# Optimization experiments

Measured on AMD Instinct MI355X. Metric: run time of the kernel, lower is better.

The kernel has to match this reference:

```python
import jax, jax.numpy as jnp
import numpy as np

B, N, C = 16, 2048, 256
C4 = C // 4
BN_EPS = 1e-5


def setup_inputs() -> dict:
    key = jax.random.key(0)
    ks = jax.random.split(key, 9)
    return {
        "x": jax.random.normal(ks[0], (B, N, C), jnp.float32),
        "Wq": jax.random.normal(ks[1], (C4, C), jnp.float32) * (1.0 / np.sqrt(C)),
        "Wk": jax.random.normal(ks[2], (C4, C), jnp.float32) * (1.0 / np.sqrt(C)),
        "Wv": jax.random.normal(ks[3], (C, C), jnp.float32) * (1.0 / np.sqrt(C)),
        "bv": jax.random.normal(ks[4], (C,), jnp.float32) * 0.01,
        "Wt": jax.random.normal(ks[5], (C, C), jnp.float32) * (1.0 / np.sqrt(C)),
        "bt": jax.random.normal(ks[6], (C,), jnp.float32) * 0.01,
        "gamma": jnp.ones((C,), jnp.float32),
        "beta": jnp.zeros((C,), jnp.float32),
        "bn_mean": jax.random.normal(ks[7], (C,), jnp.float32) * 0.1,
        "bn_var": jax.random.uniform(ks[8], (C,), jnp.float32, 0.5, 1.5),
    }


def reference(x, Wq, Wk, Wv, bv, Wt, bt, gamma, beta, bn_mean, bn_var):
    # x: (B, N, C) -> channel-first (B, C, N) as in the torch module
    xc = jnp.transpose(x, (0, 2, 1))                       # (B, C, N)
    q = jnp.einsum('oc,bcn->bno', Wq, xc)                  # (B, N, C4)
    k = jnp.einsum('oc,bcn->bon', Wk, xc)                  # (B, C4, N)
    # v_conv is computed in the original module but its output is never used;
    # it does not affect the forward output.
    energy = jnp.einsum('bno,bom->bnm', q, k)              # (B, N, N)
    attn = jax.nn.softmax(energy, axis=-1)
    # offset-attention double normalization: divide by column sums
    attn = attn / (1e-6 + jnp.sum(attn, axis=1, keepdims=True))
    x_r = jnp.einsum('bcn,bnm->bcm', xc, attn)             # (B, C, N)
    d = xc - x_r
    t = jnp.einsum('oc,bcn->bon', Wt, d) + bt[None, :, None]
    bn = gamma[None, :, None] * (t - bn_mean[None, :, None]) \
         * jax.lax.rsqrt(bn_var[None, :, None] + BN_EPS) + beta[None, :, None]
    out = xc + jnp.maximum(bn, 0.0)                        # residual + ReLU
    return jnp.transpose(out, (0, 2, 1))                   # (B, N, C)
```

## Files before the change

kernel.cpp:

```cpp
#include <hip/hip_runtime.h>
#include <math.h>
#include <stdint.h>

constexpr int B_ = 16, N_ = 2048, C_ = 256, K_ = 64;
constexpr float EPS_BN = 1e-5f;

typedef __attribute__((ext_vector_type(8))) short short8;
typedef __attribute__((ext_vector_type(16))) float f32x16;

#define MFMA32(A, Bf, Cc) __builtin_amdgcn_mfma_f32_32x32x16_bf16(A, Bf, Cc, 0, 0, 0)

constexpr size_t SZ_QK  = (size_t)B_*N_*K_*2;
constexpr size_t WSB_QH = 0;
constexpr size_t WSB_QL = WSB_QH + SZ_QK;
constexpr size_t WSB_KH = WSB_QL + SZ_QK;
constexpr size_t WSB_KL = WSB_KH + SZ_QK;
constexpr size_t WSB_Z  = WSB_KL + SZ_QK;
constexpr size_t WSB_WQT= WSB_Z  + (size_t)B_*N_*4;
constexpr size_t WSB_WKT= WSB_WQT+ (size_t)C_*K_*4;
constexpr size_t WSB_S  = WSB_WKT+ (size_t)C_*K_*4;
constexpr size_t WSB_CB = WSB_S  + (size_t)C_*4;
constexpr size_t WSB_WBH= WSB_CB + (size_t)C_*4;
constexpr size_t WSB_WBL= WSB_WBH+ (size_t)C_*C_*2;
constexpr size_t WSB_XT = (WSB_WBL + (size_t)C_*C_*2 + 255) & ~(size_t)255;
constexpr size_t XT_HALF= (size_t)B_*N_*C_*2;

__device__ inline unsigned short bf16_rne(float f) {
  uint32_t u = __float_as_uint(f);
  uint32_t r = u + 0x7FFFu + ((u >> 16) & 1u);
  return (unsigned short)(r >> 16);
}

#define GLOAD_LDS16(g, l) __builtin_amdgcn_global_load_lds( \
    (const __attribute__((address_space(1))) unsigned int*)(g), \
    (__attribute__((address_space(3))) unsigned int*)(l), 16, 0, 0)

__global__ void k0_prep(const float* __restrict__ Wq, const float* __restrict__ Wk,
                        const float* __restrict__ Wt, const float* __restrict__ bt,
                        const float* __restrict__ gamma, const float* __restrict__ beta,
                        const float* __restrict__ mean, const float* __restrict__ var,
                        char* __restrict__ ws) {
  int o = blockIdx.x, c = threadIdx.x;
  {
    float w = Wt[(size_t)o*C_ + c];
    uint32_t wb = __float_as_uint(w) & 0xFFFF0000u;
    ((unsigned short*)(ws + WSB_WBH))[(size_t)o*C_ + c] = (unsigned short)(wb >> 16);
    ((unsigned short*)(ws + WSB_WBL))[(size_t)o*C_ + c] = bf16_rne(w - __uint_as_float(wb));
  }
  if (o < K_) {
    ((float*)(ws + WSB_WQT))[(size_t)c*K_ + o] = Wq[(size_t)o*C_ + c];
    ((float*)(ws + WSB_WKT))[(size_t)c*K_ + o] = Wk[(size_t)o*C_ + c];
  }
  if (o == 0) {
    float s = gamma[c] * rsqrtf(var[c] + EPS_BN);
    ((float*)(ws + WSB_S))[c]  = s;
    ((float*)(ws + WSB_CB))[c] = s * (bt[c] - mean[c]) + beta[c];
  }
}

__global__ __launch_bounds__(256) void k1_qk(const float* __restrict__ x,
                                             char* __restrict__ ws,
                                             char* __restrict__ xtbuf) {
  __shared__ float xs[32][260];
  const float* WqT = (const float*)(ws + WSB_WQT);
  const float* WkT = (const float*)(ws + WSB_WKT);
  unsigned short* qh = (unsigned short*)(ws + WSB_QH);
  unsigned short* ql = (unsigned short*)(ws + WSB_QL);
  unsigned short* kh = (unsigned short*)(ws + WSB_KH);
  unsigned short* kl = (unsigned short*)(ws + WSB_KL);
  int b = blockIdx.x >> 6, nt = blockIdx.x & 63;
  int n0 = nt * 32, tid = threadIdx.x;

  const float4* xg = (const float4*)(x + ((size_t)b*N_ + n0)*C_);
#pragma unroll
  for (int i = 0; i < 8; i++) {
    int f = tid + i*256;
    int r = f >> 6, c4 = f & 63;
    *(float4*)&xs[r][c4*4] = xg[f];
  }
  __syncthreads();

  int o = tid & 63, rg = tid >> 6;
  float aq[8], ak[8];
#pragma unroll
  for (int j = 0; j < 8; j++) { aq[j] = 0.f; ak[j] = 0.f; }
  for (int c = 0; c < C_; c++) {
    float wq = WqT[c*K_ + o];
    float wk = WkT[c*K_ + o];
#pragma unroll
    for (int j = 0; j < 8; j++) {
      float xv = xs[rg*8 + j][c];
      aq[j] = fmaf(xv, wq, aq[j]);
      ak[j] = fmaf(xv, wk, ak[j]);
    }
  }
#pragma unroll
  for (int j = 0; j < 8; j++) {
    int n = n0 + rg*8 + j;
    size_t base = ((size_t)b*N_ + n)*K_ + o;
    float q = aq[j];
    uint32_t qb = __float_as_uint(q) & 0xFFFF0000u;
    qh[base] = (unsigned short)(qb >> 16);
    ql[base] = bf16_rne(q - __uint_as_float(qb));
    float k = ak[j];
    uint32_t kb = __float_as_uint(k) & 0xFFFF0000u;
    kh[base] = (unsigned short)(kb >> 16);
    kl[base] = bf16_rne(k - __uint_as_float(kb));
  }
#pragma unroll
  for (int nc = 0; nc < 4; nc++) {
    uint32_t hw[4], lw[4];
#pragma unroll
    for (int jj = 0; jj < 4; jj++) {
      float a  = xs[nc*8 + jj*2    ][tid];
      float bv = xs[nc*8 + jj*2 + 1][tid];
      uint32_t ab = __float_as_uint(a)  & 0xFFFF0000u;
      uint32_t bb = __float_as_uint(bv) & 0xFFFF0000u;
      hw[jj] = (ab >> 16) | bb;
      float alo = a  - __uint_as_float(ab);
      float blo = bv - __uint_as_float(bb);
      lw[jj] = (uint32_t)bf16_rne(alo) | ((uint32_t)bf16_rne(blo) << 16);
    }
    size_t toff = ((size_t)(b*64 + nt))*16384 + ((size_t)nc*256 + tid)*16;
    *(uint4*)(xtbuf + toff)           = make_uint4(hw[0], hw[1], hw[2], hw[3]);
    *(uint4*)(xtbuf + XT_HALF + toff) = make_uint4(lw[0], lw[1], lw[2], lw[3]);
  }
}

__global__ __launch_bounds__(256) void k3_stats(char* __restrict__ ws) {
  int b = blockIdx.x >> 4, nb = blockIdx.x & 15;
  int tid = threadIdx.x, wave = tid >> 6, l = tid & 63;
  int lo5 = l & 31, hi5 = l >> 5;
  int n = nb*128 + wave*32 + lo5;

  short8 qhf[4], qlf[4];
  size_t qoff = ((size_t)b*N_ + n)*K_;
#pragma unroll
  for (int cs = 0; cs < 4; cs++) {
    qhf[cs] = *(const short8*)(ws + WSB_QH + (qoff + cs*16 + hi5*8)*2);
    qlf[cs] = *(const short8*)(ws + WSB_QL + (qoff + cs*16 + hi5*8)*2);
  }
  float M = -3.0e38f, S = 0.f;
  for (int mt = 0; mt < 64; mt++) {
    size_t koff = ((size_t)b*N_ + mt*32 + lo5)*K_;
    short8 khf[4], klf[4];
#pragma unroll
    for (int cs = 0; cs < 4; cs++) {
      khf[cs] = *(const short8*)(ws + WSB_KH + (koff + cs*16 + hi5*8)*2);
      klf[cs] = *(const short8*)(ws + WSB_KL + (koff + cs*16 + hi5*8)*2);
    }
    f32x16 E = {0.f};
#pragma unroll
    for (int cs = 0; cs < 4; cs++) {
      E = MFMA32(khf[cs], qhf[cs], E);
      E = MFMA32(khf[cs], qlf[cs], E);
      E = MFMA32(klf[cs], qhf[cs], E);
    }
    float tmax = E[0];
#pragma unroll
    for (int r = 1; r < 16; r++) tmax = fmaxf(tmax, E[r]);
    float nM = fmaxf(M, tmax);
    float sc = __expf(M - nM);
    float ss = 0.f;
#pragma unroll
    for (int r = 0; r < 16; r++) ss += __expf(E[r] - nM);
    S = fmaf(S, sc, ss);
    M = nM;
  }
  float Mo = __shfl_xor(M, 32, 64);
  float So = __shfl_xor(S, 32, 64);
  float Mg = fmaxf(M, Mo);
  float Sg = S*__expf(M - Mg) + So*__expf(Mo - Mg);
  if (hi5 == 0)
    ((float*)(ws + WSB_Z))[(size_t)b*N_ + n] = Mg + __logf(Sg);
}

__global__ __launch_bounds__(256, 2) void k4_ov(const float* __restrict__ x,
                                                char* __restrict__ ws,
                                                float* __restrict__ out) {
  __shared__ __align__(16) char xtile[65536];
  __shared__ float zsb[2][32];
  __shared__ float csL[64];
  int b = blockIdx.x >> 5, mblk = blockIdx.x & 31;
  int m0 = mblk*64;
  int tid = threadIdx.x, wave = tid >> 6, l = tid & 63;
  int lo5 = l & 31, hi5 = l >> 5;
  int msub = wave >> 1, c0 = (wave & 1)*128;
  int mg = m0 + msub*32 + lo5;
  const float* Zp = (const float*)(ws + WSB_Z);
  const char* XTH = ws + WSB_XT;
  const char* XTL = ws + WSB_XT + XT_HALF;

  short8 khf[4], klf[4];
  size_t koff = ((size_t)b*N_ + mg)*K_;
#pragma unroll
  for (int cs = 0; cs < 4; cs++) {
    khf[cs] = *(const short8*)(ws + WSB_KH + (koff + cs*16 + hi5*8)*2);
    klf[cs] = *(const short8*)(ws + WSB_KL + (koff + cs*16 + hi5*8)*2);
  }
  f32x16 accO[4];
#pragma unroll
  for (int ct = 0; ct < 4; ct++) accO[ct] = (f32x16){0.f};
  float csum = 0.f;

  auto STAGE = [&](int nt, int buf) {
    size_t src = (size_t)(b*64 + nt)*16384 + (size_t)tid*16;
    char* dst = xtile + buf*32768 + tid*16;
#pragma unroll
    for (int i = 0; i < 4; i++) GLOAD_LDS16(XTH + src + (size_t)i*4096, dst + i*4096);
#pragma unroll
    for (int i = 0; i < 4; i++) GLOAD_LDS16(XTL + src + (size_t)i*4096, dst + 16384 + i*4096);
    if (tid < 32) zsb[buf][tid] = Zp[(size_t)b*N_ + nt*32 + tid];
  };
  auto QLOAD = [&](int nt, short8* qh8, short8* ql8) {
    size_t qoff2 = ((size_t)b*N_ + nt*32 + lo5)*K_;
#pragma unroll
    for (int cs = 0; cs < 4; cs++) {
      qh8[cs] = *(const short8*)(ws + WSB_QH + (qoff2 + cs*16 + hi5*8)*2);
      ql8[cs] = *(const short8*)(ws + WSB_QL + (qoff2 + cs*16 + hi5*8)*2);
    }
  };
  auto COMPUTE = [&](int buf, const short8* qh8, const short8* ql8) {
    f32x16 E = {0.f};
#pragma unroll
    for (int cs = 0; cs < 4; cs++) {
      E = MFMA32(qh8[cs], khf[cs], E);
      E = MFMA32(qh8[cs], klf[cs], E);
      E = MFMA32(ql8[cs], khf[cs], E);
    }
    float ph[16], pl[16];
#pragma unroll
    for (int r = 0; r < 16; r++) {
      int nr = (r & 3) + 8*(r >> 2) + 4*hi5;
      float p = __expf(E[r] - zsb[buf][nr]);
      csum += p;
      uint32_t pb = __float_as_uint(p) & 0xFFFF0000u;
      ph[r] = __uint_as_float(pb);
      pl[r] = p - ph[r];
    }
    uint32_t Wh[8], Wl[8];
#pragma unroll
    for (int i = 0; i < 8; i++) {
      Wh[i] = (__float_as_uint(ph[2*i]) >> 16) | (__float_as_uint(ph[2*i+1]) & 0xFFFF0000u);
      uint32_t w;
      asm("v_cvt_pk_bf16_f32 %0, %1, %2" : "=v"(w) : "v"(pl[2*i]), "v"(pl[2*i+1]));
      Wl[i] = w;
    }
    short8 pha[2], pla[2];
#pragma unroll
    for (int s = 0; s < 2; s++) {
      uint32_t a0 = Wh[s*4+0], b0 = Wh[s*4+2];
      uint32_t a1 = Wh[s*4+1], b1 = Wh[s*4+3];
      asm("v_permlane32_swap_b32 %0, %1" : "+v"(a0), "+v"(b0));
      asm("v_permlane32_swap_b32 %0, %1" : "+v"(a1), "+v"(b1));
      union { uint32_t w[4]; short8 s8; } uh;
      uh.w[0] = a0; uh.w[1] = a1; uh.w[2] = b0; uh.w[3] = b1;
      pha[s] = uh.s8;
      uint32_t c0w = Wl[s*4+0], d0 = Wl[s*4+2];
      uint32_t c1w = Wl[s*4+1], d1 = Wl[s*4+3];
      asm("v_permlane32_swap_b32 %0, %1" : "+v"(c0w), "+v"(d0));
      asm("v_permlane32_swap_b32 %0, %1" : "+v"(c1w), "+v"(d1));
      union { uint32_t w[4]; short8 s8; } ul;
      ul.w[0] = c0w; ul.w[1] = c1w; ul.w[2] = d0; ul.w[3] = d1;
      pla[s] = ul.s8;
    }
    const char* xb = xtile + buf*32768;
#pragma unroll
    for (int ct = 0; ct < 4; ct++) {
      int cc = c0 + ct*32 + lo5;
      short8 bh[2], bl[2];
#pragma unroll
      for (int ns = 0; ns < 2; ns++) {
        size_t off = ((size_t)((ns*2 + hi5)*256 + cc))*16;
        bh[ns] = *(const short8*)(xb + off);
        bl[ns] = *(const short8*)(xb + 16384 + off);
      }
#pragma unroll
      for (int ns = 0; ns < 2; ns++) {
        accO[ct] = MFMA32(pha[ns], bh[ns], accO[ct]);
        accO[ct] = MFMA32(pha[ns], bl[ns], accO[ct]);
        accO[ct] = MFMA32(pla[ns], bh[ns], accO[ct]);
      }
    }
  };

  short8 qA[4], qlA[4], qB[4], qlB[4];
  STAGE(0, 0); QLOAD(0, qA, qlA);
  __syncthreads();
  for (int base = 0; base < 64; base += 2) {
    STAGE(base + 1, 1); QLOAD(base + 1, qB, qlB);
    COMPUTE(0, qA, qlA);
    __syncthreads();
    if (base + 2 < 64) { STAGE(base + 2, 0); QLOAD(base + 2, qA, qlA); }
    COMPUTE(1, qB, qlB);
    __syncthreads();
  }

  csum += __shfl_xor(csum, 32, 64);
  if ((wave & 1) == 0 && hi5 == 0) csL[msub*32 + lo5] = csum;
  __syncthreads();
#pragma unroll
  for (int r = 0; r < 16; r++) {
    int mloc = msub*32 + (r & 3) + 8*(r >> 2) + 4*hi5;
    float ics = 1.0f / (1e-6f + csL[mloc]);
#pragma unroll
    for (int ct = 0; ct < 4; ct++) {
      int cc = c0 + ct*32 + lo5;
      float xv = x[((size_t)b*N_ + m0 + mloc)*C_ + cc];
      float dv = fmaf(-accO[ct][r], ics, xv);
      uint32_t db = __float_as_uint(dv) & 0xFFFF0000u;
      int byte = mloc*512 + ((((cc >> 3) ^ (mloc & 31)) << 4)) + ((cc & 7) << 1);
      *(unsigned short*)(xtile + byte)         = (unsigned short)(db >> 16);
      *(unsigned short*)(xtile + 32768 + byte) = bf16_rne(dv - __uint_as_float(db));
    }
  }
  __syncthreads();
  f32x16 accT[2][2];
#pragma unroll
  for (int ms = 0; ms < 2; ms++)
#pragma unroll
    for (int ot = 0; ot < 2; ot++) accT[ms][ot] = (f32x16){0.f};
#pragma unroll
  for (int cs = 0; cs < 16; cs++) {
    short8 ah[2], al[2], bh[2], bl[2];
#pragma unroll
    for (int ms = 0; ms < 2; ms++) {
      int off = (ms*32 + lo5)*512 + ((((cs*2 + hi5) ^ lo5)) << 4);
      ah[ms] = *(const short8*)(xtile + off);
      al[ms] = *(const short8*)(xtile + 32768 + off);
    }
#pragma unroll
    for (int ot = 0; ot < 2; ot++) {
      size_t wo = ((size_t)((wave*2 + ot)*32 + lo5)*C_ + cs*16 + hi5*8)*2;
      bh[ot] = *(const short8*)(ws + WSB_WBH + wo);
      bl[ot] = *(const short8*)(ws + WSB_WBL + wo);
    }
#pragma unroll
    for (int ms = 0; ms < 2; ms++)
#pragma unroll
      for (int ot = 0; ot < 2; ot++) {
        accT[ms][ot] = MFMA32(ah[ms], bh[ot], accT[ms][ot]);
        accT[ms][ot] = MFMA32(ah[ms], bl[ot], accT[ms][ot]);
        accT[ms][ot] = MFMA32(al[ms], bh[ot], accT[ms][ot]);
      }
  }
  const float* Sp = (const float*)(ws + WSB_S);
  const float* Cp = (const float*)(ws + WSB_CB);
  float sv[2], cv[2];
#pragma unroll
  for (int ot = 0; ot < 2; ot++) {
    int o = (wave*2 + ot)*32 + lo5;
    sv[ot] = Sp[o]; cv[ot] = Cp[o];
  }
#pragma unroll
  for (int ms = 0; ms < 2; ms++)
#pragma unroll
    for (int ot = 0; ot < 2; ot++)
#pragma unroll
      for (int r = 0; r < 16; r++) {
        int mloc = ms*32 + (r & 3) + 8*(r >> 2) + 4*hi5;
        int o = (wave*2 + ot)*32 + lo5;
        float bn = fmaf(sv[ot], accT[ms][ot][r], cv[ot]);
        bn = bn > 0.f ? bn : 0.f;
        size_t idx = ((size_t)b*N_ + m0 + mloc)*C_ + o;
        out[idx] = x[idx] + bn;
      }
}

extern "C" void kernel_launch(void* const* d_in, const int* in_sizes, int n_in,
                              void* d_out, int out_size, void* d_ws, size_t ws_size,
                              hipStream_t stream) {
  (void)in_sizes; (void)n_in; (void)out_size; (void)ws_size;
  const float* x     = (const float*)d_in[0];
  const float* Wq    = (const float*)d_in[1];
  const float* Wk    = (const float*)d_in[2];
  const float* Wt    = (const float*)d_in[5];
  const float* bt    = (const float*)d_in[6];
  const float* gamma = (const float*)d_in[7];
  const float* beta  = (const float*)d_in[8];
  const float* mean  = (const float*)d_in[9];
  const float* var   = (const float*)d_in[10];
  char* ws = (char*)d_ws;
  float* out = (float*)d_out;

  k0_prep <<<C_,     C_,  0, stream>>>(Wq, Wk, Wt, bt, gamma, beta, mean, var, ws);
  k1_qk   <<<B_*64,  256, 0, stream>>>(x, ws, ws + WSB_XT);
  k3_stats<<<B_*16,  256, 0, stream>>>(ws);
  k4_ov   <<<B_*32,  256, 0, stream>>>(x, ws, out);
}
```

Measured before the change: 413.8 us.

## Split stats rows across waves, read Wq/Wk rows directly, single-buffer k4 tile

k3_stats now gives each block 32 query rows and splits the 64 key tiles across the four waves, merging per-wave max and sum through shared memory. This quadruples the grid so more CUs stay busy. k1_qk reads Wq/Wk rows as float4 directly instead of a transposed copy written by k0_prep. k4_ov drops its double-buffered LDS pipeline for a single buffer with a sync before and after each load, and loses its occupancy hint. That removes load/compute overlap in the dominant kernel but may allow more occupancy.

```diff
diff --git a/kernel.cpp b/kernel.cpp
--- a/kernel.cpp
+++ b/kernel.cpp
@@ -16,9 +16,7 @@
 constexpr size_t WSB_KH = WSB_QL + SZ_QK;
 constexpr size_t WSB_KL = WSB_KH + SZ_QK;
 constexpr size_t WSB_Z  = WSB_KL + SZ_QK;
-constexpr size_t WSB_WQT= WSB_Z  + (size_t)B_*N_*4;
-constexpr size_t WSB_WKT= WSB_WQT+ (size_t)C_*K_*4;
-constexpr size_t WSB_S  = WSB_WKT+ (size_t)C_*K_*4;
+constexpr size_t WSB_S  = WSB_Z  + (size_t)B_*N_*4;
 constexpr size_t WSB_CB = WSB_S  + (size_t)C_*4;
 constexpr size_t WSB_WBH= WSB_CB + (size_t)C_*4;
 constexpr size_t WSB_WBL= WSB_WBH+ (size_t)C_*C_*2;
@@ -35,8 +33,7 @@
     (const __attribute__((address_space(1))) unsigned int*)(g), \
     (__attribute__((address_space(3))) unsigned int*)(l), 16, 0, 0)
 
-__global__ void k0_prep(const float* __restrict__ Wq, const float* __restrict__ Wk,
-                        const float* __restrict__ Wt, const float* __restrict__ bt,
+__global__ void k0_prep(const float* __restrict__ Wt, const float* __restrict__ bt,
                         const float* __restrict__ gamma, const float* __restrict__ beta,
                         const float* __restrict__ mean, const float* __restrict__ var,
                         char* __restrict__ ws) {
@@ -47,10 +44,6 @@
     ((unsigned short*)(ws + WSB_WBH))[(size_t)o*C_ + c] = (unsigned short)(wb >> 16);
     ((unsigned short*)(ws + WSB_WBL))[(size_t)o*C_ + c] = bf16_rne(w - __uint_as_float(wb));
   }
-  if (o < K_) {
-    ((float*)(ws + WSB_WQT))[(size_t)c*K_ + o] = Wq[(size_t)o*C_ + c];
-    ((float*)(ws + WSB_WKT))[(size_t)c*K_ + o] = Wk[(size_t)o*C_ + c];
-  }
   if (o == 0) {
     float s = gamma[c] * rsqrtf(var[c] + EPS_BN);
     ((float*)(ws + WSB_S))[c]  = s;
@@ -59,11 +52,11 @@
 }
 
 __global__ __launch_bounds__(256) void k1_qk(const float* __restrict__ x,
+                                             const float* __restrict__ Wq,
+                                             const float* __restrict__ Wk,
                                              char* __restrict__ ws,
                                              char* __restrict__ xtbuf) {
   __shared__ float xs[32][260];
-  const float* WqT = (const float*)(ws + WSB_WQT);
-  const float* WkT = (const float*)(ws + WSB_WKT);
   unsigned short* qh = (unsigned short*)(ws + WSB_QH);
   unsigned short* ql = (unsigned short*)(ws + WSB_QL);
   unsigned short* kh = (unsigned short*)(ws + WSB_KH);
@@ -84,14 +77,20 @@
   float aq[8], ak[8];
 #pragma unroll
   for (int j = 0; j < 8; j++) { aq[j] = 0.f; ak[j] = 0.f; }
-  for (int c = 0; c < C_; c++) {
-    float wq = WqT[c*K_ + o];
-    float wk = WkT[c*K_ + o];
+  const float4* wqr = (const float4*)(Wq + (size_t)o*C_);
+  const float4* wkr = (const float4*)(Wk + (size_t)o*C_);
+  for (int c4 = 0; c4 < 64; c4++) {
+    float4 wq4 = wqr[c4];
+    float4 wk4 = wkr[c4];
+    float4 xv[8];
+#pragma unroll
+    for (int j = 0; j < 8; j++) xv[j] = *(const float4*)&xs[rg*8 + j][c4*4];
 #pragma unroll
     for (int j = 0; j < 8; j++) {
-      float xv = xs[rg*8 + j][c];
-      aq[j] = fmaf(xv, wq, aq[j]);
-      ak[j] = fmaf(xv, wk, ak[j]);
+      aq[j] = fmaf(xv[j].x, wq4.x, aq[j]); ak[j] = fmaf(xv[j].x, wk4.x, ak[j]);
+      aq[j] = fmaf(xv[j].y, wq4.y, aq[j]); ak[j] = fmaf(xv[j].y, wk4.y, ak[j]);
+      aq[j] = fmaf(xv[j].z, wq4.z, aq[j]); ak[j] = fmaf(xv[j].z, wk4.z, ak[j]);
+      aq[j] = fmaf(xv[j].w, wq4.w, aq[j]); ak[j] = fmaf(xv[j].w, wk4.w, ak[j]);
     }
   }
 #pragma unroll
@@ -128,10 +127,11 @@
 }
 
 __global__ __launch_bounds__(256) void k3_stats(char* __restrict__ ws) {
-  int b = blockIdx.x >> 4, nb = blockIdx.x & 15;
+  __shared__ float redM[4][32], redS[4][32];
+  int b = blockIdx.x >> 6, nb = blockIdx.x & 63;
   int tid = threadIdx.x, wave = tid >> 6, l = tid & 63;
   int lo5 = l & 31, hi5 = l >> 5;
-  int n = nb*128 + wave*32 + lo5;
+  int n = nb*32 + lo5;
 
   short8 qhf[4], qlf[4];
   size_t qoff = ((size_t)b*N_ + n)*K_;
@@ -141,7 +141,7 @@
     qlf[cs] = *(const short8*)(ws + WSB_QL + (qoff + cs*16 + hi5*8)*2);
   }
   float M = -3.0e38f, S = 0.f;
-  for (int mt = 0; mt < 64; mt++) {
+  for (int mt = wave*16; mt < wave*16 + 16; mt++) {
     size_t koff = ((size_t)b*N_ + mt*32 + lo5)*K_;
     short8 khf[4], klf[4];
 #pragma unroll
@@ -171,15 +171,22 @@
   float So = __shfl_xor(S, 32, 64);
   float Mg = fmaxf(M, Mo);
   float Sg = S*__expf(M - Mg) + So*__expf(Mo - Mg);
-  if (hi5 == 0)
-    ((float*)(ws + WSB_Z))[(size_t)b*N_ + n] = Mg + __logf(Sg);
-}
-
-__global__ __launch_bounds__(256, 2) void k4_ov(const float* __restrict__ x,
-                                                char* __restrict__ ws,
-                                                float* __restrict__ out) {
+  if (hi5 == 0) { redM[wave][lo5] = Mg; redS[wave][lo5] = Sg; }
+  __syncthreads();
+  if (tid < 32) {
+    float M0 = redM[0][tid], M1 = redM[1][tid], M2 = redM[2][tid], M3 = redM[3][tid];
+    float Mt = fmaxf(fmaxf(M0, M1), fmaxf(M2, M3));
+    float St = redS[0][tid]*__expf(M0 - Mt) + redS[1][tid]*__expf(M1 - Mt)
+             + redS[2][tid]*__expf(M2 - Mt) + redS[3][tid]*__expf(M3 - Mt);
+    ((float*)(ws + WSB_Z))[(size_t)b*N_ + nb*32 + tid] = Mt + __logf(St);
+  }
+}
+
+__global__ __launch_bounds__(256) void k4_ov(const float* __restrict__ x,
+                                             char* __restrict__ ws,
+                                             float* __restrict__ out) {
   __shared__ __align__(16) char xtile[65536];
-  __shared__ float zsb[2][32];
+  __shared__ float zs[32];
   __shared__ float csL[64];
   int b = blockIdx.x >> 5, mblk = blockIdx.x & 31;
   int m0 = mblk*64;
@@ -203,24 +210,22 @@
   for (int ct = 0; ct < 4; ct++) accO[ct] = (f32x16){0.f};
   float csum = 0.f;
 
-  auto STAGE = [&](int nt, int buf) {
+  for (int nt = 0; nt < 64; nt++) {
+    __syncthreads();
     size_t src = (size_t)(b*64 + nt)*16384 + (size_t)tid*16;
-    char* dst = xtile + buf*32768 + tid*16;
-#pragma unroll
-    for (int i = 0; i < 4; i++) GLOAD_LDS16(XTH + src + (size_t)i*4096, dst + i*4096);
-#pragma unroll
-    for (int i = 0; i < 4; i++) GLOAD_LDS16(XTL + src + (size_t)i*4096, dst + 16384 + i*4096);
-    if (tid < 32) zsb[buf][tid] = Zp[(size_t)b*N_ + nt*32 + tid];
-  };
-  auto QLOAD = [&](int nt, short8* qh8, short8* ql8) {
+#pragma unroll
+    for (int i = 0; i < 4; i++) GLOAD_LDS16(XTH + src + (size_t)i*4096, xtile + tid*16 + i*4096);
+#pragma unroll
+    for (int i = 0; i < 4; i++) GLOAD_LDS16(XTL + src + (size_t)i*4096, xtile + 16384 + tid*16 + i*4096);
+    if (tid < 32) zs[tid] = Zp[(size_t)b*N_ + nt*32 + tid];
+    short8 qh8[4], ql8[4];
     size_t qoff2 = ((size_t)b*N_ + nt*32 + lo5)*K_;
 #pragma unroll
     for (int cs = 0; cs < 4; cs++) {
       qh8[cs] = *(const short8*)(ws + WSB_QH + (qoff2 + cs*16 + hi5*8)*2);
       ql8[cs] = *(const short8*)(ws + WSB_QL + (qoff2 + cs*16 + hi5*8)*2);
     }
-  };
-  auto COMPUTE = [&](int buf, const short8* qh8, const short8* ql8) {
+    __syncthreads();
     f32x16 E = {0.f};
 #pragma unroll
     for (int cs = 0; cs < 4; cs++) {
@@ -232,7 +237,7 @@
 #pragma unroll
     for (int r = 0; r < 16; r++) {
       int nr = (r & 3) + 8*(r >> 2) + 4*hi5;
-      float p = __expf(E[r] - zsb[buf][nr]);
+      float p = __expf(E[r] - zs[nr]);
       csum += p;
       uint32_t pb = __float_as_uint(p) & 0xFFFF0000u;
       ph[r] = __uint_as_float(pb);
@@ -264,7 +269,6 @@
       ul.w[0] = c0w; ul.w[1] = c1w; ul.w[2] = d0; ul.w[3] = d1;
       pla[s] = ul.s8;
     }
-    const char* xb = xtile + buf*32768;
 #pragma unroll
     for (int ct = 0; ct < 4; ct++) {
       int cc = c0 + ct*32 + lo5;
@@ -272,8 +276,8 @@
 #pragma unroll
       for (int ns = 0; ns < 2; ns++) {
         size_t off = ((size_t)((ns*2 + hi5)*256 + cc))*16;
-        bh[ns] = *(const short8*)(xb + off);
-        bl[ns] = *(const short8*)(xb + 16384 + off);
+        bh[ns] = *(const short8*)(xtile + off);
+        bl[ns] = *(const short8*)(xtile + 16384 + off);
       }
 #pragma unroll
       for (int ns = 0; ns < 2; ns++) {
@@ -282,18 +286,6 @@
         accO[ct] = MFMA32(pla[ns], bh[ns], accO[ct]);
       }
     }
-  };
-
-  short8 qA[4], qlA[4], qB[4], qlB[4];
-  STAGE(0, 0); QLOAD(0, qA, qlA);
-  __syncthreads();
-  for (int base = 0; base < 64; base += 2) {
-    STAGE(base + 1, 1); QLOAD(base + 1, qB, qlB);
-    COMPUTE(0, qA, qlA);
-    __syncthreads();
-    if (base + 2 < 64) { STAGE(base + 2, 0); QLOAD(base + 2, qA, qlA); }
-    COMPUTE(1, qB, qlB);
-    __syncthreads();
   }
 
   csum += __shfl_xor(csum, 32, 64);
@@ -383,8 +375,8 @@
   char* ws = (char*)d_ws;
   float* out = (float*)d_out;
 
-  k0_prep <<<C_,     C_,  0, stream>>>(Wq, Wk, Wt, bt, gamma, beta, mean, var, ws);
-  k1_qk   <<<B_*64,  256, 0, stream>>>(x, ws, ws + WSB_XT);
-  k3_stats<<<B_*16,  256, 0, stream>>>(ws);
+  k0_prep <<<C_,     C_,  0, stream>>>(Wt, bt, gamma, beta, mean, var, ws);
+  k1_qk   <<<B_*64,  256, 0, stream>>>(x, Wq, Wk, ws, ws + WSB_XT);
+  k3_stats<<<B_*64,  256, 0, stream>>>(ws);
   k4_ov   <<<B_*32,  256, 0, stream>>>(x, ws, out);
 }
```

After: 415.9 us. No clear change (+0.5%).
